# Optimization experiments

Hardware: AMD Instinct MI355X
Metric: run time of the kernel (lower is better)

The kernel has to match this reference:

```python
import jax, jax.numpy as jnp
import numpy as np

LMBDA = 0.95
RHO_MAX = 1.0
C_MAX = 1.0
N, T = 8192, 1024


def setup_inputs() -> dict:
    key = jax.random.key(0)
    ks = jax.random.split(key, 7)
    gammas = jax.random.uniform(ks[0], (N, T), dtype=jnp.float32) * 0.02 + 0.97  # discounts near 0.99
    vf_x = jax.random.normal(ks[1], (N, T + 1), dtype=jnp.float32)
    rewards = jax.random.normal(ks[2], (N, T), dtype=jnp.float32)
    action_lls = jax.random.normal(ks[3], (N, T), dtype=jnp.float32) * 0.1
    original_action_lls = jax.random.normal(ks[4], (N, T), dtype=jnp.float32) * 0.1
    terminated = jax.random.randint(ks[5], (N,), 0, 2) > 0
    episode_lengths = jax.random.randint(ks[6], (N,), 1, T + 1)
    return {
        "gammas": gammas,
        "vf_x": vf_x,
        "rewards": rewards,
        "action_lls": action_lls,
        "original_action_lls": original_action_lls,
        "terminated": terminated,
        "episode_lengths": episode_lengths,
    }


def reference(gammas, vf_x, rewards, action_lls, original_action_lls, terminated, episode_lengths):
    n_episodes, max_len = rewards.shape
    importance_weight = jnp.exp(action_lls - original_action_lls)
    rho = jnp.minimum(importance_weight, RHO_MAX)
    ep_idx = jnp.arange(n_episodes)
    # zero out discount at final step of terminated episodes
    gammas = gammas.at[ep_idx, episode_lengths - 1].multiply((~terminated).astype(gammas.dtype))
    c = LMBDA * jnp.minimum(importance_weight, C_MAX)
    gamma_c = gammas * c  # (N, T)
    delta_V = rho * (rewards + gammas * vf_x[:, 1:] - vf_x[:, :-1])  # (N, T)

    # backward recurrence: v_diff[t] = delta_V[t] + gamma_c[t] * v_diff[t+1], v_diff[T] = 0
    def step(carry, inp):
        dV_t, gc_t = inp  # each (N,)
        v = dV_t + gc_t * carry
        return v, v

    init = jnp.zeros((n_episodes,), dtype=vf_x.dtype)
    _, ys = jax.lax.scan(step, init, (delta_V.T[::-1], gamma_c.T[::-1]))  # ys: (T, N) reversed time
    v_diff = jnp.concatenate([ys[::-1].T, jnp.zeros((n_episodes, 1), dtype=vf_x.dtype)], axis=1)  # (N, T+1)
    v_s = v_diff + vf_x
    advantages = rho * (rewards * gammas * v_s[:, 1:] - vf_x[:, :-1])
    return advantages, v_s
```

## Files before the change

kernel.cpp:

```cpp
#include <hip/hip_runtime.h>

static constexpr int N_EP  = 8192;
static constexpr int T_LEN = 1024;
static constexpr float LMBDA = 0.95f;

__global__ __launch_bounds__(256) void vtrace_kernel(
    const float* __restrict__ gammas,
    const float* __restrict__ vf_x,
    const float* __restrict__ rewards,
    const float* __restrict__ action_lls,
    const float* __restrict__ orig_lls,
    const int*   __restrict__ terminated,
    const int*   __restrict__ ep_len,
    float* __restrict__ adv_out,
    float* __restrict__ vs_out)
{
    const int n    = blockIdx.x * 4 + (threadIdx.x >> 6);
    const int lane = threadIdx.x & 63;
    if (n >= N_EP) return;

    const long rowT  = (long)n * T_LEN;
    const long rowT1 = (long)n * (T_LEN + 1);
    const int  term  = terminated[n];
    const int  kill  = ep_len[n] - 1;

    float v_in = 0.0f;

#pragma unroll
    for (int q = 3; q >= 0; --q) {
        const int base = q * 256 + lane * 4;

        const float4 gg = *reinterpret_cast<const float4*>(gammas     + rowT + base);
        const float4 rr = *reinterpret_cast<const float4*>(rewards    + rowT + base);
        const float4 aa = *reinterpret_cast<const float4*>(action_lls + rowT + base);
        const float4 oo = *reinterpret_cast<const float4*>(orig_lls   + rowT + base);
        float g[4] = {gg.x, gg.y, gg.z, gg.w};
        float r[4] = {rr.x, rr.y, rr.z, rr.w};
        float rho[4];
        rho[0] = fminf(__expf(aa.x - oo.x), 1.0f);
        rho[1] = fminf(__expf(aa.y - oo.y), 1.0f);
        rho[2] = fminf(__expf(aa.z - oo.z), 1.0f);
        rho[3] = fminf(__expf(aa.w - oo.w), 1.0f);

        float vf[5];
#pragma unroll
        for (int k = 0; k < 5; ++k) vf[k] = vf_x[rowT1 + base + k];

        if (term) {
#pragma unroll
            for (int j = 0; j < 4; ++j)
                if (kill == base + j) g[j] = 0.0f;
        }

        float A = 1.0f, B = 0.0f;
#pragma unroll
        for (int j = 3; j >= 0; --j) {
            const float gc = LMBDA * rho[j] * g[j];
            const float dv = rho[j] * fmaf(g[j], vf[j + 1], r[j] - vf[j]);
            B = fmaf(gc, B, dv);
            A *= gc;
        }

#pragma unroll
        for (int d = 1; d < 64; d <<= 1) {
            const float An = __shfl_down(A, d, 64);
            const float Bn = __shfl_down(B, d, 64);
            if (lane + d < 64) { B = fmaf(A, Bn, B); A *= An; }
        }
        const float A1 = __shfl_down(A, 1, 64);
        const float B1 = __shfl_down(B, 1, 64);
        const float carry = (lane == 63) ? v_in : fmaf(A1, v_in, B1);

        float vs_next = carry + vf[4];
        if (q == 3 && lane == 63)
            vs_out[rowT1 + T_LEN] = vs_next;

        float v = carry;
        float vsa[4], adv[4];
#pragma unroll
        for (int j = 3; j >= 0; --j) {
            const float gc = LMBDA * rho[j] * g[j];
            const float dv = rho[j] * fmaf(g[j], vf[j + 1], r[j] - vf[j]);
            v = fmaf(gc, v, dv);
            vsa[j] = v + vf[j];
            adv[j] = rho[j] * fmaf(r[j] * g[j], vs_next, -vf[j]);
            vs_next = vsa[j];
        }

        *reinterpret_cast<float4*>(adv_out + rowT + base) =
            make_float4(adv[0], adv[1], adv[2], adv[3]);
#pragma unroll
        for (int j = 0; j < 4; ++j) vs_out[rowT1 + base + j] = vsa[j];

        v_in = __shfl(v, 0, 64);
    }
}

extern "C" void kernel_launch(void* const* d_in, const int* in_sizes, int n_in,
                              void* d_out, int out_size, void* d_ws, size_t ws_size,
                              hipStream_t stream) {
    const float* gammas     = (const float*)d_in[0];
    const float* vf_x       = (const float*)d_in[1];
    const float* rewards    = (const float*)d_in[2];
    const float* action_lls = (const float*)d_in[3];
    const float* orig_lls   = (const float*)d_in[4];
    const int*   terminated = (const int*)d_in[5];
    const int*   ep_len     = (const int*)d_in[6];

    float* adv = (float*)d_out;
    float* vs  = adv + (long)N_EP * T_LEN;

    dim3 grid(N_EP / 4), block(256);
    hipLaunchKernelGGL(vtrace_kernel, grid, block, 0, stream,
                       gammas, vf_x, rewards, action_lls, orig_lls,
                       terminated, ep_len, adv, vs);
}
```

Baseline: 40.58 us.

## Hoist all loads, scan four chunks together, and use nontemporal stores

All four 256-element chunks of each row are now loaded up front, and the four wavefront scans run interleaved. The carry between chunks is chained through lane-0 aggregates instead of running each chunk's scan serially after the previous one. Outputs are written with nontemporal stores. This is meant to expose more memory-level parallelism and hide shuffle latency, at the cost of much higher register pressure and possibly lower occupancy.

Result: no change. 41.11 us (+1.3%).

```diff
diff --git a/kernel.cpp b/kernel.cpp
--- a/kernel.cpp
+++ b/kernel.cpp
@@ -3,6 +3,8 @@
 static constexpr int N_EP  = 8192;
 static constexpr int T_LEN = 1024;
 static constexpr float LMBDA = 0.95f;
+
+typedef float floatx4 __attribute__((ext_vector_type(4)));
 
 __global__ __launch_bounds__(256) void vtrace_kernel(
     const float* __restrict__ gammas,
@@ -17,82 +19,110 @@
 {
     const int n    = blockIdx.x * 4 + (threadIdx.x >> 6);
     const int lane = threadIdx.x & 63;
-    if (n >= N_EP) return;
-
     const long rowT  = (long)n * T_LEN;
     const long rowT1 = (long)n * (T_LEN + 1);
-    const int  term  = terminated[n];
-    const int  kill  = ep_len[n] - 1;
 
-    float v_in = 0.0f;
+    floatx4 gg[4], rr[4], aa[4], oo[4];
+    float vf[4][5];
+#pragma unroll
+    for (int q = 0; q < 4; ++q) {
+        const int base = q * 256 + lane * 4;
+        gg[q] = *reinterpret_cast<const floatx4*>(gammas     + rowT + base);
+        rr[q] = *reinterpret_cast<const floatx4*>(rewards    + rowT + base);
+        aa[q] = *reinterpret_cast<const floatx4*>(action_lls + rowT + base);
+        oo[q] = *reinterpret_cast<const floatx4*>(orig_lls   + rowT + base);
+    }
+#pragma unroll
+    for (int q = 0; q < 4; ++q) {
+        const int base = q * 256 + lane * 4;
+#pragma unroll
+        for (int k = 0; k < 5; ++k) vf[q][k] = vf_x[rowT1 + base + k];
+    }
+    const int term = terminated[n];
+    const int kill = ep_len[n] - 1;
+
+    float g[4][4], r[4][4], rho[4][4];
+#pragma unroll
+    for (int q = 0; q < 4; ++q) {
+#pragma unroll
+        for (int j = 0; j < 4; ++j) {
+            g[q][j] = gg[q][j];
+            r[q][j] = rr[q][j];
+            rho[q][j] = fminf(__expf(aa[q][j] - oo[q][j]), 1.0f);
+        }
+        if (term) {
+            const int base = q * 256 + lane * 4;
+#pragma unroll
+            for (int j = 0; j < 4; ++j)
+                if (kill == base + j) g[q][j] = 0.0f;
+        }
+    }
+
+    float A[4], B[4];
+#pragma unroll
+    for (int q = 0; q < 4; ++q) {
+        float Aq = 1.0f, Bq = 0.0f;
+#pragma unroll
+        for (int j = 3; j >= 0; --j) {
+            const float gc = LMBDA * rho[q][j] * g[q][j];
+            const float dv = rho[q][j] * fmaf(g[q][j], vf[q][j + 1], r[q][j] - vf[q][j]);
+            Bq = fmaf(gc, Bq, dv);
+            Aq *= gc;
+        }
+        A[q] = Aq; B[q] = Bq;
+    }
+
+#pragma unroll
+    for (int d = 1; d < 64; d <<= 1) {
+#pragma unroll
+        for (int q = 0; q < 4; ++q) {
+            const float An = __shfl_down(A[q], d, 64);
+            const float Bn = __shfl_down(B[q], d, 64);
+            if (lane + d < 64) { B[q] = fmaf(A[q], Bn, B[q]); A[q] *= An; }
+        }
+    }
+    float A1[4], B1[4], A0[4], B0[4];
+#pragma unroll
+    for (int q = 0; q < 4; ++q) {
+        A1[q] = __shfl_down(A[q], 1, 64);
+        B1[q] = __shfl_down(B[q], 1, 64);
+        A0[q] = __shfl(A[q], 0, 64);
+        B0[q] = __shfl(B[q], 0, 64);
+    }
+
+    float v_in[4];
+    v_in[3] = 0.0f;
+    v_in[2] = B0[3];
+    v_in[1] = fmaf(A0[2], v_in[2], B0[2]);
+    v_in[0] = fmaf(A0[1], v_in[1], B0[1]);
 
 #pragma unroll
     for (int q = 3; q >= 0; --q) {
         const int base = q * 256 + lane * 4;
-
-        const float4 gg = *reinterpret_cast<const float4*>(gammas     + rowT + base);
-        const float4 rr = *reinterpret_cast<const float4*>(rewards    + rowT + base);
-        const float4 aa = *reinterpret_cast<const float4*>(action_lls + rowT + base);
-        const float4 oo = *reinterpret_cast<const float4*>(orig_lls   + rowT + base);
-        float g[4] = {gg.x, gg.y, gg.z, gg.w};
-        float r[4] = {rr.x, rr.y, rr.z, rr.w};
-        float rho[4];
-        rho[0] = fminf(__expf(aa.x - oo.x), 1.0f);
-        rho[1] = fminf(__expf(aa.y - oo.y), 1.0f);
-        rho[2] = fminf(__expf(aa.z - oo.z), 1.0f);
-        rho[3] = fminf(__expf(aa.w - oo.w), 1.0f);
-
-        float vf[5];
-#pragma unroll
-        for (int k = 0; k < 5; ++k) vf[k] = vf_x[rowT1 + base + k];
-
-        if (term) {
-#pragma unroll
-            for (int j = 0; j < 4; ++j)
-                if (kill == base + j) g[j] = 0.0f;
-        }
-
-        float A = 1.0f, B = 0.0f;
-#pragma unroll
-        for (int j = 3; j >= 0; --j) {
-            const float gc = LMBDA * rho[j] * g[j];
-            const float dv = rho[j] * fmaf(g[j], vf[j + 1], r[j] - vf[j]);
-            B = fmaf(gc, B, dv);
-            A *= gc;
-        }
-
-#pragma unroll
-        for (int d = 1; d < 64; d <<= 1) {
-            const float An = __shfl_down(A, d, 64);
-            const float Bn = __shfl_down(B, d, 64);
-            if (lane + d < 64) { B = fmaf(A, Bn, B); A *= An; }
-        }
-        const float A1 = __shfl_down(A, 1, 64);
-        const float B1 = __shfl_down(B, 1, 64);
-        const float carry = (lane == 63) ? v_in : fmaf(A1, v_in, B1);
-
-        float vs_next = carry + vf[4];
+        const float carry = (lane == 63) ? v_in[q]
+                                         : fmaf(A1[q], v_in[q], B1[q]);
+        float vs_next = carry + vf[q][4];
         if (q == 3 && lane == 63)
-            vs_out[rowT1 + T_LEN] = vs_next;
+            __builtin_nontemporal_store(vs_next, vs_out + rowT1 + T_LEN);
 
         float v = carry;
         float vsa[4], adv[4];
 #pragma unroll
         for (int j = 3; j >= 0; --j) {
-            const float gc = LMBDA * rho[j] * g[j];
-            const float dv = rho[j] * fmaf(g[j], vf[j + 1], r[j] - vf[j]);
+            const float gc = LMBDA * rho[q][j] * g[q][j];
+            const float dv = rho[q][j] * fmaf(g[q][j], vf[q][j + 1], r[q][j] - vf[q][j]);
             v = fmaf(gc, v, dv);
-            vsa[j] = v + vf[j];
-            adv[j] = rho[j] * fmaf(r[j] * g[j], vs_next, -vf[j]);
+            vsa[j] = v + vf[q][j];
+            adv[j] = rho[q][j] * fmaf(r[q][j] * g[q][j], vs_next, -vf[q][j]);
             vs_next = vsa[j];
         }
 
-        *reinterpret_cast<float4*>(adv_out + rowT + base) =
-            make_float4(adv[0], adv[1], adv[2], adv[3]);
+        floatx4 av; av[0] = adv[0]; av[1] = adv[1]; av[2] = adv[2]; av[3] = adv[3];
+        __builtin_nontemporal_store(
+            av, reinterpret_cast<floatx4*>(adv_out + rowT + base));
 #pragma unroll
-        for (int j = 0; j < 4; ++j) vs_out[rowT1 + base + j] = vsa[j];
-
-        v_in = __shfl(v, 0, 64);
+        for (int j = 0; j < 4; ++j)
+            __builtin_nontemporal_store(vsa[j], vs_out + rowT1 + base + j);
     }
 }
 
```
